# Performance work log

Measured on AMD Instinct MI355X. Metric: run time of the kernel, lower is better.

Reference implementation:

```python
import jax, jax.numpy as jnp
import numpy as np

N = 50000      # number of nodes (src == dst, homogeneous block)
E = 800000     # number of edges
H = 2          # num_heads
D = 32         # out_dim per head
IN = 64        # target input feature dim
DMID = 64      # 'mid' node-type feature dim
EREL = 200000  # size of 'rel' edge feature table
DREL = 32      # 'rel' edge feature dim
ED = 2 * D     # edge_dim (concat of mid + rel virtual feats per head)


def setup_inputs() -> dict:
    key = jax.random.key(0)
    ks = jax.random.split(key, 18)
    s = 0.05
    return {
        "h": jax.random.normal(ks[0], (N, IN), jnp.float32),
        "W_t": jax.random.normal(ks[1], (IN, H * D), jnp.float32) * s,
        "b_t": jax.random.normal(ks[2], (H * D,), jnp.float32) * s,
        "nfeat_mid": jax.random.normal(ks[3], (N, DMID), jnp.float32),
        "W_mid": jax.random.normal(ks[4], (DMID, H * D), jnp.float32) * s,
        "b_mid": jax.random.normal(ks[5], (H * D,), jnp.float32) * s,
        "efeat_rel": jax.random.normal(ks[6], (EREL, DREL), jnp.float32),
        "W_rel": jax.random.normal(ks[7], (DREL, H * D), jnp.float32) * s,
        "b_rel": jax.random.normal(ks[8], (H * D,), jnp.float32) * s,
        "attn_src": jax.random.normal(ks[9], (1, H, D), jnp.float32) * s,
        "attn_dst": jax.random.normal(ks[10], (1, H, D), jnp.float32) * s,
        "attn_edge": jax.random.normal(ks[11], (1, H, ED), jnp.float32) * s,
        "W_edge": jax.random.normal(ks[12], (ED, D), jnp.float32) * s,
        "b_edge": jax.random.normal(ks[13], (D,), jnp.float32) * s,
        "src_idx": jax.random.randint(ks[14], (E,), 0, N, jnp.int32),
        "dst_idx": jax.random.randint(ks[15], (E,), 0, N, jnp.int32),
        "hn": jax.random.randint(ks[16], (E, 1), 0, N, jnp.int32),
        "he": jax.random.randint(ks[17], (E, 1), 0, EREL, jnp.int32),
    }


def reference(h, W_t, b_t, nfeat_mid, W_mid, b_mid, efeat_rel, W_rel, b_rel,
              attn_src, attn_dst, attn_edge, W_edge, b_edge,
              src_idx, dst_idx, hn, he):
    # target node projection -> [N, H, D]
    hp = (h @ W_t + b_t).reshape(-1, H, D)
    # per-node attention logits (GAT style) -> [N, H]
    e_src = jnp.sum(attn_src * jax.nn.relu(hp), axis=-1)
    e_dst = jnp.sum(attn_dst * jax.nn.relu(hp), axis=-1)
    # per-edge logits: u_add_v -> [E, H]
    e = e_src[src_idx] + e_dst[dst_idx]

    # virtual edge features gathered along metapath: [E, H, 2D]
    hn_f = (nfeat_mid @ W_mid + b_mid).reshape(-1, H, D)[hn[:, 0]]
    he_f = (efeat_rel @ W_rel + b_rel).reshape(-1, H, D)[he[:, 0]]
    h_e = jnp.concatenate([hn_f, he_f], axis=-1)
    e = e + jnp.sum(attn_edge * jax.nn.relu(h_e), axis=-1)

    # edge_softmax: segment softmax over incoming edges of each dst node
    m = jax.ops.segment_max(e, dst_idx, num_segments=N)
    m = jnp.where(jnp.isfinite(m), m, 0.0)  # zero-degree nodes
    ex = jnp.exp(e - m[dst_idx])
    denom = jax.ops.segment_sum(ex, dst_idx, num_segments=N)
    a = ex / denom[dst_idx]                  # [E, H]

    # u_mul_e scatter-sum aggregation -> [N, H, D]
    rst = jax.ops.segment_sum(hp[src_idx] * a[..., None], dst_idx, num_segments=N)
    # edge-feature aggregation -> [N, H, 2D], then fc_edge
    ft2 = jax.ops.segment_sum(h_e * a[..., None], dst_idx, num_segments=N)
    rst = rst + ft2 @ W_edge + b_edge

    # residual + activation
    rst = jax.nn.relu(rst + hp)
    out = rst.reshape(N, H * D)
    # l2 normalize (F.normalize, eps=1e-12)
    out = out / jnp.maximum(jnp.linalg.norm(out, axis=1, keepdims=True), 1e-12)
    return out
```

## Files before the change

### kernel.cpp

```cpp
#include <hip/hip_runtime.h>

typedef unsigned int uint;
#define LOG2E 1.4426950408889634f

__device__ __forceinline__ float bf16_lo(uint v) { return __uint_as_float(v << 16); }
__device__ __forceinline__ float bf16_hi(uint v) { return __uint_as_float(v & 0xffff0000u); }
__device__ __forceinline__ unsigned short f2bf(float f) {
    uint u = __float_as_uint(f);
    return (unsigned short)((u + 0x7fffu + ((u >> 16) & 1u)) >> 16);
}
__device__ __forceinline__ float bf16u(uint s) {
    return __uint_as_float(s << 16);
}

template<int K>
__device__ __forceinline__ void proj_body(
    int blk, const float* __restrict__ X, const float* __restrict__ W,
    const float* __restrict__ bias, const float* __restrict__ avec0,
    const float* __restrict__ avec1, int mode, int nrows,
    float* __restrict__ outF32, unsigned short* __restrict__ outF16,
    float2* __restrict__ outA0, float2* __restrict__ outA1,
    float* Xsh, float* av0sh, float* av1sh, float* bsh)
{
    constexpr int XP = 68;
    int t = threadIdx.x;

    if (t < 64) {
        int head = t >> 5, d = t & 31;
        int aidx = (mode == 0) ? t : (mode == 1 ? head * 64 + d : head * 64 + 32 + d);
        av0sh[t] = avec0 ? avec0[aidx] : 0.f;
        av1sh[t] = avec1 ? avec1[aidx] : 0.f;
        bsh[t] = bias[t];
    }

    int base = blk * 64;
    const float4* X4 = (const float4*)X;
    for (int i = t; i < 64 * (K / 4); i += 256) {
        int row = i / (K / 4), c4 = i % (K / 4);
        int gr = base + row; if (gr >= nrows) gr = nrows - 1;
        *(float4*)&Xsh[row * XP + c4 * 4] = X4[(size_t)gr * (K / 4) + c4];
    }
    __syncthreads();

    const float4* __restrict__ W4 = (const float4*)W;
    int rquad = t >> 4, cq = t & 15;
    float acc[4][4];
#pragma unroll
    for (int ri = 0; ri < 4; ++ri)
#pragma unroll
        for (int ci = 0; ci < 4; ++ci) acc[ri][ci] = 0.f;

#pragma unroll 4
    for (int kq = 0; kq < K / 4; ++kq) {
        float4 wq0 = W4[(4 * kq + 0) * 16 + cq];
        float4 wq1 = W4[(4 * kq + 1) * 16 + cq];
        float4 wq2 = W4[(4 * kq + 2) * 16 + cq];
        float4 wq3 = W4[(4 * kq + 3) * 16 + cq];
#pragma unroll
        for (int ri = 0; ri < 4; ++ri) {
            float4 xq = *(const float4*)&Xsh[(4 * rquad + ri) * XP + 4 * kq];
            acc[ri][0] += xq.x * wq0.x + xq.y * wq1.x + xq.z * wq2.x + xq.w * wq3.x;
            acc[ri][1] += xq.x * wq0.y + xq.y * wq1.y + xq.z * wq2.y + xq.w * wq3.y;
            acc[ri][2] += xq.x * wq0.z + xq.y * wq1.z + xq.z * wq2.z + xq.w * wq3.z;
            acc[ri][3] += xq.x * wq0.w + xq.y * wq1.w + xq.z * wq2.w + xq.w * wq3.w;
        }
    }

    int c0 = cq * 4;
    float4 bv  = *(float4*)&bsh[c0];
    float4 a0v = *(float4*)&av0sh[c0];
    float4 a1v = *(float4*)&av1sh[c0];
    float4 vv[4];
    float s0[4], s1[4];
#pragma unroll
    for (int ri = 0; ri < 4; ++ri) {
        float4 val;
        val.x = acc[ri][0] + bv.x;
        val.y = acc[ri][1] + bv.y;
        val.z = acc[ri][2] + bv.z;
        val.w = acc[ri][3] + bv.w;
        vv[ri] = val;
        float r0 = fmaxf(val.x, 0.f), r1 = fmaxf(val.y, 0.f);
        float r2 = fmaxf(val.z, 0.f), r3 = fmaxf(val.w, 0.f);
        s0[ri] = r0 * a0v.x + r1 * a0v.y + r2 * a0v.z + r3 * a0v.w;
        s1[ri] = r0 * a1v.x + r1 * a1v.y + r2 * a1v.z + r3 * a1v.w;
    }
#pragma unroll
    for (int ri = 0; ri < 4; ++ri) {
        s0[ri] += __shfl_xor(s0[ri], 1, 64);
        s0[ri] += __shfl_xor(s0[ri], 2, 64);
        s0[ri] += __shfl_xor(s0[ri], 4, 64);
        s1[ri] += __shfl_xor(s1[ri], 1, 64);
        s1[ri] += __shfl_xor(s1[ri], 2, 64);
        s1[ri] += __shfl_xor(s1[ri], 4, 64);
    }
    float s0x[4], s1x[4];
#pragma unroll
    for (int ri = 0; ri < 4; ++ri) {
        s0x[ri] = __shfl_xor(s0[ri], 8, 64);
        s1x[ri] = __shfl_xor(s1[ri], 8, 64);
    }

    int rbase = base + rquad * 4;
#pragma unroll
    for (int ri = 0; ri < 4; ++ri) {
        int row = rbase + ri;
        if (row >= nrows) continue;
        if (outF32)
            *(float4*)&outF32[(size_t)row * 64 + c0] = vv[ri];
        uint u0 = (uint)f2bf(vv[ri].x) | ((uint)f2bf(vv[ri].y) << 16);
        uint u1 = (uint)f2bf(vv[ri].z) | ((uint)f2bf(vv[ri].w) << 16);
        *(uint2*)&outF16[(size_t)row * 64 + c0] = make_uint2(u0, u1);
        if (cq == 0 && outA0)
            outA0[row] = make_float2(s0[ri] * LOG2E, s0x[ri] * LOG2E);
        if (cq == 1 && outA1)
            outA1[row] = make_float2(s1[ri] * LOG2E, s1x[ri] * LOG2E);
    }
}

__global__ __launch_bounds__(256) void mega_kernel(
    const float* __restrict__ h, const float* __restrict__ W_t, const float* __restrict__ b_t,
    const float* __restrict__ nfeat_mid, const float* __restrict__ W_mid, const float* __restrict__ b_mid,
    const float* __restrict__ efeat_rel, const float* __restrict__ W_rel, const float* __restrict__ b_rel,
    const float* __restrict__ attn_src, const float* __restrict__ attn_dst, const float* __restrict__ attn_edge,
    const int* __restrict__ dst_idx, int* __restrict__ deg,
    float* __restrict__ hp32, unsigned short* __restrict__ hp16,
    unsigned short* __restrict__ mid16, unsigned short* __restrict__ rel16,
    float2* __restrict__ e_src, float2* __restrict__ e_dst,
    float2* __restrict__ em, float2* __restrict__ er,
    int N, int EREL, int E, int nC, int nA, int nB)
{
    __shared__ float Xsh[64 * 68];
    __shared__ float av0sh[64], av1sh[64], bsh[64];
    int b = blockIdx.x;
    if (b < nC) {
        proj_body<32>(b, efeat_rel, W_rel, b_rel, attn_edge, nullptr, 2, EREL,
                      nullptr, rel16, er, nullptr, Xsh, av0sh, av1sh, bsh);
    } else if (b < nC + nA) {
        proj_body<64>(b - nC, h, W_t, b_t, attn_src, attn_dst, 0, N,
                      hp32, hp16, e_src, e_dst, Xsh, av0sh, av1sh, bsh);
    } else if (b < nC + nA + nB) {
        proj_body<64>(b - nC - nA, nfeat_mid, W_mid, b_mid, attn_edge, nullptr, 1, N,
                      nullptr, mid16, em, nullptr, Xsh, av0sh, av1sh, bsh);
    } else {
        int i = (b - nC - nA - nB) * 256 + threadIdx.x;
        if (i < E) atomicAdd(&deg[dst_idx[i]], 1);
    }
}

__global__ __launch_bounds__(256) void scanA_kernel(
    const int* __restrict__ deg, int* __restrict__ blkSums, int N)
{
    __shared__ int red[256];
    int t = threadIdx.x;
    int base = blockIdx.x * 1024 + t * 4;
    int s = 0;
    if (base + 3 < N) {
        int4 v = *(const int4*)&deg[base];
        s = v.x + v.y + v.z + v.w;
    } else {
        for (int i = 0; i < 4; ++i) if (base + i < N) s += deg[base + i];
    }
    red[t] = s;
    __syncthreads();
    for (int off = 128; off >= 1; off >>= 1) {
        if (t < off) red[t] += red[t + off];
        __syncthreads();
    }
    if (t == 0) blkSums[blockIdx.x] = red[0];
}

__global__ __launch_bounds__(256) void scanC_kernel(
    const int* __restrict__ deg, const int* __restrict__ blkSums,
    int* __restrict__ row_ptr, int* __restrict__ cursor, int N, int nblk)
{
    __shared__ int sh[256];
    __shared__ int blkOffSh;
    int t = threadIdx.x;
    int blk = blockIdx.x;
    int base = blk * 1024 + t * 4;

    if (t < 64) {
        int s = 0;
        for (int j = t; j < blk; j += 64) s += blkSums[j];
        for (int m = 32; m >= 1; m >>= 1) s += __shfl_xor(s, m, 64);
        if (t == 0) blkOffSh = s;
    }

    int4 v = make_int4(0, 0, 0, 0);
    if (base + 3 < N) v = *(const int4*)&deg[base];
    else {
        if (base < N)     v.x = deg[base];
        if (base + 1 < N) v.y = deg[base + 1];
        if (base + 2 < N) v.z = deg[base + 2];
    }
    int ts = v.x + v.y + v.z + v.w;
    sh[t] = ts;
    __syncthreads();
    for (int off = 1; off < 256; off <<= 1) {
        int val = (t >= off) ? sh[t - off] : 0;
        __syncthreads();
        sh[t] += val;
        __syncthreads();
    }
    int blkOff = blkOffSh;
    int ex = blkOff + ((t == 0) ? 0 : sh[t - 1]);
    int p0 = ex, p1 = ex + v.x, p2 = p1 + v.y, p3 = p2 + v.z;
    if (base < N)     { row_ptr[base]     = p0; cursor[base]     = p0; }
    if (base + 1 < N) { row_ptr[base + 1] = p1; cursor[base + 1] = p1; }
    if (base + 2 < N) { row_ptr[base + 2] = p2; cursor[base + 2] = p2; }
    if (base + 3 < N) { row_ptr[base + 3] = p3; cursor[base + 3] = p3; }
    if (blk == nblk - 1 && t == 255) row_ptr[N] = blkOff + sh[255];
}

__global__ __launch_bounds__(256) void scatter_kernel(
    const int* __restrict__ src, const int* __restrict__ dst,
    const int* __restrict__ hn, const int* __restrict__ he,
    const float2* __restrict__ es, const float2* __restrict__ ed,
    const float2* __restrict__ em, const float2* __restrict__ er,
    int* __restrict__ cursor, uint4* __restrict__ erec, int E)
{
    int i = blockIdx.x * blockDim.x + threadIdx.x;
    if (i >= E) return;
    int s = src[i], d = dst[i], a = hn[i], b = he[i];
    float2 v1 = es[s], v2 = ed[d], v3 = em[a], v4 = er[b];
    float e0 = fminf(fmaxf(v1.x + v2.x + v3.x + v4.x, -60.f), 60.f);
    float e1 = fminf(fmaxf(v1.y + v2.y + v3.y + v4.y, -60.f), 60.f);
    int pos = atomicAdd(&cursor[d], 1);
    erec[pos] = make_uint4((uint)s | ((uint)a << 16), (uint)b,
                           __float_as_uint(e0), __float_as_uint(e1));
}

__global__ __launch_bounds__(256) void aggregate_kernel(
    const int* __restrict__ row_ptr, const uint4* __restrict__ erec,
    const float* __restrict__ hp32,
    const unsigned short* __restrict__ hp16,
    const unsigned short* __restrict__ mid16,
    const unsigned short* __restrict__ rel16,
    const float* __restrict__ We, const float* __restrict__ be,
    float* __restrict__ out, int N)
{
    __shared__ float WeSh[64 * 32];
    __shared__ float ft2sh[4][128];
    int t = threadIdx.x;
    for (int i = t; i < 64 * 32; i += 256) WeSh[i] = We[i];
    __syncthreads();

    int wave = t >> 6, lane = t & 63;
    int head = lane >> 5, dj = lane & 31;
    int n = blockIdx.x * 4 + wave;
    bool valid = n < N;
    int nn = valid ? n : 0;

    int start = row_ptr[nn], end = row_ptr[nn + 1];
    int cnt = end - start;
    int lenA = cnt >> 1;
    int midp = start + lenA;

    bool isrel = lane >= 32;
    int l31 = lane & 31;
    bool h1w = ((lane >> 4) & 1) != 0;
    const uint* tab32 = (const uint*)(isrel ? rel16 : mid16);

    float rstcA = 0.f, fxA = 0.f, fyA = 0.f, den0A = 0.f, den1A = 0.f;
    float rstcB = 0.f, fxB = 0.f, fyB = 0.f, den0B = 0.f, den1B = 0.f;

#pragma unroll 2
    for (int k = 0; k < lenA; ++k) {
        uint4 rA = erec[start + k];
        uint4 rB = erec[midp + k];
        uint huA = (uint)hp16[((rA.x & 0xffffu) << 6) | (uint)lane];
        uint huB = (uint)hp16[((rB.x & 0xffffu) << 6) | (uint)lane];
        uint pvA = tab32[((isrel ? rA.y : (rA.x >> 16)) << 5) | (uint)l31];
        uint pvB = tab32[((isrel ? rB.y : (rB.x >> 16)) << 5) | (uint)l31];

        float a0A = __builtin_amdgcn_exp2f(__uint_as_float(rA.z));
        float a1A = __builtin_amdgcn_exp2f(__uint_as_float(rA.w));
        den0A += a0A; den1A += a1A;
        rstcA += bf16u(huA) * (head ? a1A : a0A);
        float wA = h1w ? a1A : a0A;
        fxA += bf16_lo(pvA) * wA;
        fyA += bf16_hi(pvA) * wA;

        float a0B = __builtin_amdgcn_exp2f(__uint_as_float(rB.z));
        float a1B = __builtin_amdgcn_exp2f(__uint_as_float(rB.w));
        den0B += a0B; den1B += a1B;
        rstcB += bf16u(huB) * (head ? a1B : a0B);
        float wB = h1w ? a1B : a0B;
        fxB += bf16_lo(pvB) * wB;
        fyB += bf16_hi(pvB) * wB;
    }
    if (cnt & 1) {
        uint4 rB = erec[end - 1];
        uint huB = (uint)hp16[((rB.x & 0xffffu) << 6) | (uint)lane];
        uint pvB = tab32[((isrel ? rB.y : (rB.x >> 16)) << 5) | (uint)l31];
        float a0B = __builtin_amdgcn_exp2f(__uint_as_float(rB.z));
        float a1B = __builtin_amdgcn_exp2f(__uint_as_float(rB.w));
        den0B += a0B; den1B += a1B;
        rstcB += bf16u(huB) * (head ? a1B : a0B);
        float wB = h1w ? a1B : a0B;
        fxB += bf16_lo(pvB) * wB;
        fyB += bf16_hi(pvB) * wB;
    }

    float den0 = den0A + den0B, den1 = den1A + den1B;
    float rstc = rstcA + rstcB, fx = fxA + fxB, fy = fyA + fyB;

    float inv0 = den0 > 0.f ? 1.f / den0 : 0.f;
    float inv1 = den1 > 0.f ? 1.f / den1 : 0.f;
    rstc *= head ? inv1 : inv0;
    float invf = h1w ? inv1 : inv0;

    int slotbase;
    if (lane < 16)      slotbase = 2 * lane;
    else if (lane < 32) slotbase = 2 * lane + 32;
    else if (lane < 48) slotbase = 2 * lane - 32;
    else                slotbase = 2 * lane;
    ft2sh[wave][slotbase]     = fx * invf;
    ft2sh[wave][slotbase + 1] = fy * invf;

    __builtin_amdgcn_sched_barrier(0);
    asm volatile("s_waitcnt lgkmcnt(0)" ::: "memory");
    __builtin_amdgcn_sched_barrier(0);

    float fc = be[dj];
#pragma unroll 8
    for (int dd = 0; dd < 64; ++dd)
        fc += ft2sh[wave][head * 64 + dd] * WeSh[dd * 32 + dj];

    float val = rstc + fc + hp32[(uint)nn * 64 + lane];
    val = fmaxf(val, 0.f);

    float ss = val * val;
    for (int m = 32; m >= 1; m >>= 1) ss += __shfl_xor(ss, m, 64);
    float invn = 1.f / fmaxf(sqrtf(ss), 1e-12f);
    if (valid) out[(uint)nn * 64 + lane] = val * invn;
}

extern "C" void kernel_launch(void* const* d_in, const int* in_sizes, int n_in,
                              void* d_out, int out_size, void* d_ws, size_t ws_size,
                              hipStream_t stream)
{
    const float* h         = (const float*)d_in[0];
    const float* W_t       = (const float*)d_in[1];
    const float* b_t       = (const float*)d_in[2];
    const float* nfeat_mid = (const float*)d_in[3];
    const float* W_mid     = (const float*)d_in[4];
    const float* b_mid     = (const float*)d_in[5];
    const float* efeat_rel = (const float*)d_in[6];
    const float* W_rel     = (const float*)d_in[7];
    const float* b_rel     = (const float*)d_in[8];
    const float* attn_src  = (const float*)d_in[9];
    const float* attn_dst  = (const float*)d_in[10];
    const float* attn_edge = (const float*)d_in[11];
    const float* W_edge    = (const float*)d_in[12];
    const float* b_edge    = (const float*)d_in[13];
    const int* src_idx     = (const int*)d_in[14];
    const int* dst_idx     = (const int*)d_in[15];
    const int* hn          = (const int*)d_in[16];
    const int* he          = (const int*)d_in[17];
    float* out = (float*)d_out;

    const int N    = in_sizes[0] / 64;
    const int EREL = in_sizes[6] / 32;
    const int E    = in_sizes[14];

    char* ws = (char*)d_ws;
    auto alloc = [&](size_t bytes) {
        void* p = (void*)ws;
        ws += (bytes + 255) & ~(size_t)255;
        return p;
    };
    float* hp32           = (float*)alloc((size_t)N * 64 * 4);
    unsigned short* hp16  = (unsigned short*)alloc((size_t)N * 64 * 2);
    unsigned short* mid16 = (unsigned short*)alloc((size_t)N * 64 * 2);
    unsigned short* rel16 = (unsigned short*)alloc((size_t)EREL * 64 * 2);
    float2* e_src  = (float2*)alloc((size_t)N * 8);
    float2* e_dst  = (float2*)alloc((size_t)N * 8);
    float2* em     = (float2*)alloc((size_t)N * 8);
    float2* er     = (float2*)alloc((size_t)EREL * 8);
    int* deg       = (int*)alloc((size_t)N * 4);
    int* row_ptr   = (int*)alloc((size_t)(N + 1) * 4);
    int* cursor    = (int*)alloc((size_t)N * 4);
    int* blkSums   = (int*)alloc((size_t)64 * 4);
    uint4* erec    = (uint4*)alloc((size_t)E * 16);

    hipMemsetAsync(deg, 0, (size_t)N * 4, stream);

    int nA = (N + 63) / 64;
    int nB = nA;
    int nC = (EREL + 63) / 64;
    int nD = (E + 255) / 256;
    mega_kernel<<<nC + nA + nB + nD, 256, 0, stream>>>(
        h, W_t, b_t, nfeat_mid, W_mid, b_mid, efeat_rel, W_rel, b_rel,
        attn_src, attn_dst, attn_edge, dst_idx, deg,
        hp32, hp16, mid16, rel16, e_src, e_dst, em, er,
        N, EREL, E, nC, nA, nB);

    int nblk = (N + 1023) / 1024;
    scanA_kernel<<<nblk, 256, 0, stream>>>(deg, blkSums, N);
    scanC_kernel<<<nblk, 256, 0, stream>>>(deg, blkSums, row_ptr, cursor, N, nblk);

    scatter_kernel<<<(E + 255) / 256, 256, 0, stream>>>(
        src_idx, dst_idx, hn, he, e_src, e_dst, em, er, cursor, erec, E);

    aggregate_kernel<<<(N + 3) / 4, 256, 0, stream>>>(
        row_ptr, erec, hp32, hp16, mid16, rel16, W_edge, b_edge, out, N);
}
```

Measured before the change: 301.9 us.

## Compute node/edge projections with bf16 MFMA and drop fp32 hp copy

Replaces the scalar FMA projection GEMMs with bf16 MFMA 16x16x32 instructions. Inputs and the transposed weights are converted to bf16 in shared memory, and the attention logits are reduced through lane shuffles. The fp32 copy of the target projection is removed, so the residual in the aggregate kernel reads the bf16 copy instead. This cuts ALU work and memory writes in the projection stage. The cost is lower precision in the projection and the residual, and each block repeats the weight transpose.

```diff
diff --git a/kernel.cpp b/kernel.cpp
--- a/kernel.cpp
+++ b/kernel.cpp
@@ -1,6 +1,8 @@
 #include <hip/hip_runtime.h>
 
 typedef unsigned int uint;
+typedef float f32x4 __attribute__((ext_vector_type(4)));
+typedef short short8 __attribute__((ext_vector_type(8)));
 #define LOG2E 1.4426950408889634f
 
 __device__ __forceinline__ float bf16_lo(uint v) { return __uint_as_float(v << 16); }
@@ -14,15 +16,16 @@
 }
 
 template<int K>
-__device__ __forceinline__ void proj_body(
+__device__ __forceinline__ void proj_mfma(
     int blk, const float* __restrict__ X, const float* __restrict__ W,
     const float* __restrict__ bias, const float* __restrict__ avec0,
     const float* __restrict__ avec1, int mode, int nrows,
-    float* __restrict__ outF32, unsigned short* __restrict__ outF16,
+    unsigned short* __restrict__ outF16,
     float2* __restrict__ outA0, float2* __restrict__ outA1,
-    float* Xsh, float* av0sh, float* av1sh, float* bsh)
-{
-    constexpr int XP = 68;
+    unsigned short* Xbf, unsigned short* WT,
+    float* av0sh, float* av1sh, float* bsh)
+{
+    constexpr int KP = K + 8;
     int t = threadIdx.x;
 
     if (t < 64) {
@@ -34,87 +37,74 @@
     }
 
     int base = blk * 64;
+    constexpr int FP4R = K / 4;
     const float4* X4 = (const float4*)X;
-    for (int i = t; i < 64 * (K / 4); i += 256) {
-        int row = i / (K / 4), c4 = i % (K / 4);
+    for (int f = t; f < 64 * FP4R; f += 256) {
+        int row = f / FP4R, c4 = f % FP4R;
         int gr = base + row; if (gr >= nrows) gr = nrows - 1;
-        *(float4*)&Xsh[row * XP + c4 * 4] = X4[(size_t)gr * (K / 4) + c4];
+        float4 v = X4[(size_t)gr * FP4R + c4];
+        uint2 u;
+        u.x = (uint)f2bf(v.x) | ((uint)f2bf(v.y) << 16);
+        u.y = (uint)f2bf(v.z) | ((uint)f2bf(v.w) << 16);
+        *(uint2*)&Xbf[row * KP + c4 * 4] = u;
+    }
+    const float4* W4 = (const float4*)W;
+    for (int f = t; f < K * 16; f += 256) {
+        int k = f >> 4, c4 = (f & 15) * 4;
+        float4 v = W4[f];
+        WT[(c4 + 0) * KP + k] = f2bf(v.x);
+        WT[(c4 + 1) * KP + k] = f2bf(v.y);
+        WT[(c4 + 2) * KP + k] = f2bf(v.z);
+        WT[(c4 + 3) * KP + k] = f2bf(v.w);
     }
     __syncthreads();
 
-    const float4* __restrict__ W4 = (const float4*)W;
-    int rquad = t >> 4, cq = t & 15;
-    float acc[4][4];
-#pragma unroll
-    for (int ri = 0; ri < 4; ++ri)
-#pragma unroll
-        for (int ci = 0; ci < 4; ++ci) acc[ri][ci] = 0.f;
-
-#pragma unroll 4
-    for (int kq = 0; kq < K / 4; ++kq) {
-        float4 wq0 = W4[(4 * kq + 0) * 16 + cq];
-        float4 wq1 = W4[(4 * kq + 1) * 16 + cq];
-        float4 wq2 = W4[(4 * kq + 2) * 16 + cq];
-        float4 wq3 = W4[(4 * kq + 3) * 16 + cq];
-#pragma unroll
-        for (int ri = 0; ri < 4; ++ri) {
-            float4 xq = *(const float4*)&Xsh[(4 * rquad + ri) * XP + 4 * kq];
-            acc[ri][0] += xq.x * wq0.x + xq.y * wq1.x + xq.z * wq2.x + xq.w * wq3.x;
-            acc[ri][1] += xq.x * wq0.y + xq.y * wq1.y + xq.z * wq2.y + xq.w * wq3.y;
-            acc[ri][2] += xq.x * wq0.z + xq.y * wq1.z + xq.z * wq2.z + xq.w * wq3.z;
-            acc[ri][3] += xq.x * wq0.w + xq.y * wq1.w + xq.z * wq2.w + xq.w * wq3.w;
+    int w = t >> 6, l = t & 63;
+    int l15 = l & 15, kg = l >> 4;
+
+    short8 a[K / 32];
+#pragma unroll
+    for (int ks = 0; ks < K / 32; ++ks)
+        a[ks] = *(const short8*)&Xbf[(16 * w + l15) * KP + ks * 32 + kg * 8];
+
+    f32x4 acc[4];
+#pragma unroll
+    for (int c = 0; c < 4; ++c) {
+        acc[c] = (f32x4){0.f, 0.f, 0.f, 0.f};
+#pragma unroll
+        for (int ks = 0; ks < K / 32; ++ks) {
+            short8 b = *(const short8*)&WT[(16 * c + l15) * KP + ks * 32 + kg * 8];
+            acc[c] = __builtin_amdgcn_mfma_f32_16x16x32_bf16(a[ks], b, acc[c], 0, 0, 0);
         }
     }
 
-    int c0 = cq * 4;
-    float4 bv  = *(float4*)&bsh[c0];
-    float4 a0v = *(float4*)&av0sh[c0];
-    float4 a1v = *(float4*)&av1sh[c0];
-    float4 vv[4];
-    float s0[4], s1[4];
-#pragma unroll
-    for (int ri = 0; ri < 4; ++ri) {
-        float4 val;
-        val.x = acc[ri][0] + bv.x;
-        val.y = acc[ri][1] + bv.y;
-        val.z = acc[ri][2] + bv.z;
-        val.w = acc[ri][3] + bv.w;
-        vv[ri] = val;
-        float r0 = fmaxf(val.x, 0.f), r1 = fmaxf(val.y, 0.f);
-        float r2 = fmaxf(val.z, 0.f), r3 = fmaxf(val.w, 0.f);
-        s0[ri] = r0 * a0v.x + r1 * a0v.y + r2 * a0v.z + r3 * a0v.w;
-        s1[ri] = r0 * a1v.x + r1 * a1v.y + r2 * a1v.z + r3 * a1v.w;
-    }
-#pragma unroll
-    for (int ri = 0; ri < 4; ++ri) {
-        s0[ri] += __shfl_xor(s0[ri], 1, 64);
-        s0[ri] += __shfl_xor(s0[ri], 2, 64);
-        s0[ri] += __shfl_xor(s0[ri], 4, 64);
-        s1[ri] += __shfl_xor(s1[ri], 1, 64);
-        s1[ri] += __shfl_xor(s1[ri], 2, 64);
-        s1[ri] += __shfl_xor(s1[ri], 4, 64);
-    }
-    float s0x[4], s1x[4];
-#pragma unroll
-    for (int ri = 0; ri < 4; ++ri) {
-        s0x[ri] = __shfl_xor(s0[ri], 8, 64);
-        s1x[ri] = __shfl_xor(s1[ri], 8, 64);
-    }
-
-    int rbase = base + rquad * 4;
-#pragma unroll
-    for (int ri = 0; ri < 4; ++ri) {
-        int row = rbase + ri;
-        if (row >= nrows) continue;
-        if (outF32)
-            *(float4*)&outF32[(size_t)row * 64 + c0] = vv[ri];
-        uint u0 = (uint)f2bf(vv[ri].x) | ((uint)f2bf(vv[ri].y) << 16);
-        uint u1 = (uint)f2bf(vv[ri].z) | ((uint)f2bf(vv[ri].w) << 16);
-        *(uint2*)&outF16[(size_t)row * 64 + c0] = make_uint2(u0, u1);
-        if (cq == 0 && outA0)
-            outA0[row] = make_float2(s0[ri] * LOG2E, s0x[ri] * LOG2E);
-        if (cq == 1 && outA1)
-            outA1[row] = make_float2(s1[ri] * LOG2E, s1x[ri] * LOG2E);
+#pragma unroll
+    for (int r = 0; r < 4; ++r) {
+        int grow = base + 16 * w + 4 * kg + r;
+        bool rok = grow < nrows;
+        float p00 = 0.f, p01 = 0.f, p10 = 0.f, p11 = 0.f;
+#pragma unroll
+        for (int c = 0; c < 4; ++c) {
+            int col = 16 * c + l15;
+            float val = acc[c][r] + bsh[col];
+            if (rok) outF16[(size_t)grow * 64 + col] = f2bf(val);
+            float rl = fmaxf(val, 0.f);
+            float q0 = av0sh[col] * rl, q1 = av1sh[col] * rl;
+            if (c < 2) { p00 += q0; p10 += q1; }
+            else       { p01 += q0; p11 += q1; }
+        }
+        p00 += __shfl_xor(p00, 1, 64); p00 += __shfl_xor(p00, 2, 64);
+        p00 += __shfl_xor(p00, 4, 64); p00 += __shfl_xor(p00, 8, 64);
+        p01 += __shfl_xor(p01, 1, 64); p01 += __shfl_xor(p01, 2, 64);
+        p01 += __shfl_xor(p01, 4, 64); p01 += __shfl_xor(p01, 8, 64);
+        p10 += __shfl_xor(p10, 1, 64); p10 += __shfl_xor(p10, 2, 64);
+        p10 += __shfl_xor(p10, 4, 64); p10 += __shfl_xor(p10, 8, 64);
+        p11 += __shfl_xor(p11, 1, 64); p11 += __shfl_xor(p11, 2, 64);
+        p11 += __shfl_xor(p11, 4, 64); p11 += __shfl_xor(p11, 8, 64);
+        if (l15 == 0 && rok) {
+            outA0[grow] = make_float2(p00 * LOG2E, p01 * LOG2E);
+            if (outA1) outA1[grow] = make_float2(p10 * LOG2E, p11 * LOG2E);
+        }
     }
 }
 
@@ -124,24 +114,25 @@
     const float* __restrict__ efeat_rel, const float* __restrict__ W_rel, const float* __restrict__ b_rel,
     const float* __restrict__ attn_src, const float* __restrict__ attn_dst, const float* __restrict__ attn_edge,
     const int* __restrict__ dst_idx, int* __restrict__ deg,
-    float* __restrict__ hp32, unsigned short* __restrict__ hp16,
+    unsigned short* __restrict__ hp16,
     unsigned short* __restrict__ mid16, unsigned short* __restrict__ rel16,
     float2* __restrict__ e_src, float2* __restrict__ e_dst,
     float2* __restrict__ em, float2* __restrict__ er,
     int N, int EREL, int E, int nC, int nA, int nB)
 {
-    __shared__ float Xsh[64 * 68];
+    __shared__ unsigned short Xbf[64 * 72];
+    __shared__ unsigned short WT[64 * 72];
     __shared__ float av0sh[64], av1sh[64], bsh[64];
     int b = blockIdx.x;
     if (b < nC) {
-        proj_body<32>(b, efeat_rel, W_rel, b_rel, attn_edge, nullptr, 2, EREL,
-                      nullptr, rel16, er, nullptr, Xsh, av0sh, av1sh, bsh);
+        proj_mfma<32>(b, efeat_rel, W_rel, b_rel, attn_edge, nullptr, 2, EREL,
+                      rel16, er, nullptr, Xbf, WT, av0sh, av1sh, bsh);
     } else if (b < nC + nA) {
-        proj_body<64>(b - nC, h, W_t, b_t, attn_src, attn_dst, 0, N,
-                      hp32, hp16, e_src, e_dst, Xsh, av0sh, av1sh, bsh);
+        proj_mfma<64>(b - nC, h, W_t, b_t, attn_src, attn_dst, 0, N,
+                      hp16, e_src, e_dst, Xbf, WT, av0sh, av1sh, bsh);
     } else if (b < nC + nA + nB) {
-        proj_body<64>(b - nC - nA, nfeat_mid, W_mid, b_mid, attn_edge, nullptr, 1, N,
-                      nullptr, mid16, em, nullptr, Xsh, av0sh, av1sh, bsh);
+        proj_mfma<64>(b - nC - nA, nfeat_mid, W_mid, b_mid, attn_edge, nullptr, 1, N,
+                      mid16, em, nullptr, Xbf, WT, av0sh, av1sh, bsh);
     } else {
         int i = (b - nC - nA - nB) * 256 + threadIdx.x;
         if (i < E) atomicAdd(&deg[dst_idx[i]], 1);
@@ -233,7 +224,6 @@
 
 __global__ __launch_bounds__(256) void aggregate_kernel(
     const int* __restrict__ row_ptr, const uint4* __restrict__ erec,
-    const float* __restrict__ hp32,
     const unsigned short* __restrict__ hp16,
     const unsigned short* __restrict__ mid16,
     const unsigned short* __restrict__ rel16,
@@ -328,7 +318,7 @@
     for (int dd = 0; dd < 64; ++dd)
         fc += ft2sh[wave][head * 64 + dd] * WeSh[dd * 32 + dj];
 
-    float val = rstc + fc + hp32[(uint)nn * 64 + lane];
+    float val = rstc + fc + bf16u((uint)hp16[(uint)nn * 64 + (uint)lane]);
     val = fmaxf(val, 0.f);
 
     float ss = val * val;
@@ -371,7 +361,6 @@
         ws += (bytes + 255) & ~(size_t)255;
         return p;
     };
-    float* hp32           = (float*)alloc((size_t)N * 64 * 4);
     unsigned short* hp16  = (unsigned short*)alloc((size_t)N * 64 * 2);
     unsigned short* mid16 = (unsigned short*)alloc((size_t)N * 64 * 2);
     unsigned short* rel16 = (unsigned short*)alloc((size_t)EREL * 64 * 2);
@@ -394,7 +383,7 @@
     mega_kernel<<<nC + nA + nB + nD, 256, 0, stream>>>(
         h, W_t, b_t, nfeat_mid, W_mid, b_mid, efeat_rel, W_rel, b_rel,
         attn_src, attn_dst, attn_edge, dst_idx, deg,
-        hp32, hp16, mid16, rel16, e_src, e_dst, em, er,
+        hp16, mid16, rel16, e_src, e_dst, em, er,
         N, EREL, E, nC, nA, nB);
 
     int nblk = (N + 1023) / 1024;
@@ -405,5 +394,5 @@
         src_idx, dst_idx, hn, he, e_src, e_dst, em, er, cursor, erec, E);
 
     aggregate_kernel<<<(N + 3) / 4, 256, 0, stream>>>(
-        row_ptr, erec, hp32, hp16, mid16, rel16, W_edge, b_edge, out, N);
-}
+        row_ptr, erec, hp16, mid16, rel16, W_edge, b_edge, out, N);
+}
```

Result: faster. 282.3 us (-6.5%).
